# Optimization experiments

Measured on AMD Instinct MI355X. Metric: run time of the kernel, lower is better.

Reference implementation:

```python
import jax, jax.numpy as jnp
import numpy as np

M = 16384          # test points
N = 16384          # train points
D = 2              # (kx, ky)
CHUNK = 8192       # rows of K_star per chunk (matches torch default)


def setup_inputs() -> dict:
    key = jax.random.key(0)
    k1, k2, k3 = jax.random.split(key, 3)
    X_test = jax.random.normal(k1, (M, D), dtype=jnp.float32)
    X_train = jax.random.normal(k2, (N, D), dtype=jnp.float32)
    alpha = jax.random.normal(k3, (N, 2), dtype=jnp.float32)  # dual vars [Re, Im]
    log_lengthscale = jnp.asarray(np.log(0.1), dtype=jnp.float32)
    log_outputscale = jnp.asarray(np.log(1.0), dtype=jnp.float32)
    return {
        "X_test": X_test,
        "X_train": X_train,
        "alpha": alpha,
        "log_lengthscale": log_lengthscale,
        "log_outputscale": log_outputscale,
    }


def reference(X_test, X_train, alpha, log_lengthscale, log_outputscale):
    """Posterior mean mu* = K_rbf(X_test, X_train) @ alpha, chunked over test rows."""
    ell2 = jnp.exp(log_lengthscale) ** 2
    sf2 = jnp.exp(log_outputscale) ** 2
    xt_sq = jnp.sum(X_train * X_train, axis=1)  # (N,)

    def chunk_fn(xc):  # xc: (CHUNK, D)
        # squared euclidean distances (clamped at 0 for numerical safety)
        sq = (jnp.sum(xc * xc, axis=1)[:, None]
              + xt_sq[None, :]
              - 2.0 * (xc @ X_train.T))          # (CHUNK, N)
        sq = jnp.maximum(sq, 0.0)
        K = sf2 * jnp.exp(-0.5 * sq / ell2)      # RBF kernel values
        return K @ alpha                          # (CHUNK, 2)

    m = X_test.shape[0]
    chunks = X_test.reshape(m // CHUNK, CHUNK, D)
    out = jax.lax.map(chunk_fn, chunks)           # (m//CHUNK, CHUNK, 2)
    return out.reshape(m, 2)
```

## Files before the change

kernel.cpp:

```cpp
#include <hip/hip_runtime.h>
#include <math.h>

#define M_PTS 16384
#define N_PTS 16384

#define NC 42
#define NCELLS (NC * NC)
#define NPAIR (NCELLS / 2)
#define H 0.25f
#define INV_H 4.0f
#define ORIG (-5.25f)
#define TCUT 20.0f
#define KMAX 7
#define MAXROWS 16
#define NWAVES (M_PTS / 64)
#define CHUNK 1024
#define MAX_ITEMS 4096

#define OFF_NITEMS 0
#define OFF_TRCUR 64
#define OFF_TECUR (OFF_TRCUR + NCELLS * 4)
#define OFF_SROW  (OFF_TECUR + NCELLS * 4)
#define OFF_SPRE  (OFF_SROW + NWAVES * MAXROWS * 4)
#define OFF_ITEMS (OFF_SPRE + NWAVES * (MAXROWS + 1) * 4)
#define OFF_TRA   ((OFF_ITEMS + MAX_ITEMS * 4 + 255) & ~255)
#define OFF_TRW1  (OFF_TRA + N_PTS * 16)
#define OFF_T4    (OFF_TRW1 + N_PTS * 4)
#define WS_NEED   (OFF_T4 + (size_t)M_PTS * 16)

__device__ __forceinline__ float fexp2(float x) {
#if __has_builtin(__builtin_amdgcn_exp2f)
    return __builtin_amdgcn_exp2f(x);
#else
    return exp2f(x);
#endif
}

__device__ __forceinline__ void gatomic_fadd(float* p, float v) {
    asm volatile("global_atomic_add_f32 %0, %1, off" :: "v"(p), "v"(v) : "memory");
}

__device__ __forceinline__ int cellco(float v) {
    int c = (int)floorf((v - ORIG) * INV_H);
    return min(NC - 1, max(0, c));
}

__global__ __launch_bounds__(1024) void prep_kernel(
        const float2* __restrict__ Xtr, const float2* __restrict__ Xte,
        const float* __restrict__ log_ell,
        int* __restrict__ trcur, int* __restrict__ tecur,
        int* __restrict__ sRowG, int* __restrict__ sPreG,
        int* __restrict__ items, int* __restrict__ nitemsG) {
    __shared__ int hTr[NCELLS], hTe[NCELLS];
    __shared__ int sc[1024];
    __shared__ int trsL[NCELLS + 1], PL[NCELLS + 1];
    const int tid = threadIdx.x;

    if (tid == 0) nitemsG[0] = 0;
    for (int i = tid; i < NCELLS; i += 1024) { hTr[i] = 0; hTe[i] = 0; }
    __syncthreads();
    for (int i = tid; i < N_PTS; i += 1024) {
        float2 t = Xtr[i];
        atomicAdd(&hTr[cellco(t.y) * NC + cellco(t.x)], 1);
        float2 x = Xte[i];
        atomicAdd(&hTe[cellco(x.y) * NC + cellco(x.x)], 1);
    }
    __syncthreads();

    int pv = (tid < NPAIR) ? (hTr[2 * tid] + hTr[2 * tid + 1]) : 0;
    sc[tid] = pv; __syncthreads();
    for (int off = 1; off < 1024; off <<= 1) {
        int u = (tid >= off) ? sc[tid - off] : 0;
        __syncthreads(); sc[tid] += u; __syncthreads();
    }
    if (tid < NPAIR) {
        int e = sc[tid] - pv;
        trsL[2 * tid] = e;
        trsL[2 * tid + 1] = e + hTr[2 * tid];
    }
    if (tid == NPAIR - 1) trsL[NCELLS] = sc[tid];
    __syncthreads();

    pv = (tid < NPAIR) ? (hTe[2 * tid] + hTe[2 * tid + 1]) : 0;
    sc[tid] = pv; __syncthreads();
    for (int off = 1; off < 1024; off <<= 1) {
        int u = (tid >= off) ? sc[tid - off] : 0;
        __syncthreads(); sc[tid] += u; __syncthreads();
    }
    if (tid < NPAIR) {
        int e = sc[tid] - pv;
        PL[2 * tid] = e;
        PL[2 * tid + 1] = e + hTe[2 * tid];
    }
    if (tid == NPAIR - 1) PL[NCELLS] = sc[tid];
    __syncthreads();

    for (int c = tid; c < NCELLS; c += 1024) {
        trcur[c] = trsL[c];
        tecur[c] = PL[c];
    }

    if (tid < NWAVES) {
        const int w = tid;
        const float ell = expf(log_ell[0]);
        const float cmag = 0.5f / (ell * ell) * 1.4426950408889634f;
        const float r2 = TCUT / cmag;
        const int K = (int)floorf(sqrtf(r2) * INV_H) + 1;

        int clo, chi;
        {
            int s = w * 64, lo = 0, hi = NCELLS;
            while (lo + 1 < hi) { int m = (lo + hi) >> 1; if (PL[m] <= s) lo = m; else hi = m; }
            clo = lo;
            s = w * 64 + 63; lo = 0; hi = NCELLS;
            while (lo + 1 < hi) { int m = (lo + hi) >> 1; if (PL[m] <= s) lo = m; else hi = m; }
            chi = lo;
        }
        const int rl = clo / NC, cl = clo % NC;
        const int rh = chi / NC, ch = chi % NC;
        int wlo = max(0, rl - K), whi = min(NC - 1, rh + K);
        int nr = whi - wlo + 1;
        bool full = (K > KMAX) || (nr > MAXROWS);

        int pre = 0;
        if (full) {
            sRowG[w * MAXROWS] = 0;
            sPreG[w * (MAXROWS + 1)] = 0;
            pre = N_PTS;
            for (int i = 1; i <= MAXROWS; ++i) sPreG[w * (MAXROWS + 1) + i] = N_PTS;
        } else {
            const bool single = (rl == rh);
            const int cmin = single ? cl : 0;
            const int cmax = single ? ch : (NC - 1);
            sPreG[w * (MAXROWS + 1)] = 0;
            int idx = 0;
            for (int wr = wlo; wr <= whi; ++wr, ++idx) {
                int dy = (wr < rl) ? (rl - wr) : ((wr > rh) ? (wr - rh) : 0);
                int kx;
                if (dy <= 1) kx = K;
                else {
                    float d = (float)(dy - 1) * H;
                    kx = (int)floorf(sqrtf(fmaxf(r2 - d * d, 0.f)) * INV_H) + 1;
                }
                int c0 = max(0, cmin - kx);
                int c1 = min(NC - 1, cmax + kx);
                int js = trsL[wr * NC + c0];
                int je = trsL[wr * NC + c1 + 1];
                sRowG[w * MAXROWS + idx] = js - pre;
                pre += je - js;
                sPreG[w * (MAXROWS + 1) + idx + 1] = pre;
            }
            for (; idx < MAXROWS; ++idx)
                sPreG[w * (MAXROWS + 1) + idx + 1] = pre;
        }
        const int nch = (pre + CHUNK - 1) / CHUNK;
        for (int k = 0; k < nch; ++k) {
            int slot = atomicAdd(nitemsG, 1);
            items[slot] = w | (k << 16);
        }
    }
}

__global__ void scatter_kernel(const float2* __restrict__ Xtr,
                               const float2* __restrict__ Xte,
                               const float2* __restrict__ alpha,
                               const float* __restrict__ log_ell,
                               const float* __restrict__ log_sf,
                               int* __restrict__ trcur, int* __restrict__ tecur,
                               float4* __restrict__ trA, float* __restrict__ trW1,
                               float4* __restrict__ T4, float2* __restrict__ out2) {
    int i = blockIdx.x * blockDim.x + threadIdx.x;
    if (i >= N_PTS) return;
    out2[i] = make_float2(0.f, 0.f);
    float ell = expf(log_ell[0]);
    float sf2 = expf(2.0f * log_sf[0]);
    float c = -0.5f / (ell * ell) * 1.4426950408889634f;

    float2 t = Xtr[i];
    float2 a = alpha[i];
    int ct = cellco(t.y) * NC + cellco(t.x);
    int pt = atomicAdd(&trcur[ct], 1);
    trA[pt] = make_float4(-2.f * c * t.x, -2.f * c * t.y,
                          c * (t.x * t.x + t.y * t.y), sf2 * a.x);
    trW1[pt] = sf2 * a.y;

    float2 x = Xte[i];
    int cx = cellco(x.y) * NC + cellco(x.x);
    int px = atomicAdd(&tecur[cx], 1);
    T4[px] = make_float4(x.x, x.y, c * (x.x * x.x + x.y * x.y),
                         __int_as_float(i));
}

__global__ __launch_bounds__(256) void gp_main(
        const float4* __restrict__ T4, const float4* __restrict__ trA,
        const float* __restrict__ trW1, const int* __restrict__ sRowG,
        const int* __restrict__ sPreG, const int* __restrict__ items,
        const int* __restrict__ nitemsG, float* __restrict__ out) {
    const int nit = nitemsG[0];
    if ((int)blockIdx.x >= nit) return;
    const int item = items[blockIdx.x];
    const int w = item & 0xFFFF;
    const int k = item >> 16;

    __shared__ float4 sA[CHUNK];
    __shared__ __align__(16) float sW[CHUNK];
    __shared__ float2 red[4][64];
    __shared__ int off[MAXROWS];
    __shared__ int pre[MAXROWS + 1];

    const int tid = threadIdx.x;
    const int p = tid >> 6;
    const int lane = tid & 63;

    if (tid < MAXROWS) off[tid] = sRowG[w * MAXROWS + tid];
    if (tid < MAXROWS + 1) pre[tid] = sPreG[w * (MAXROWS + 1) + tid];

    float4 tp = T4[w * 64 + lane];
    const float x = tp.x, y = tp.y, b = tp.z;
    const int oi = __float_as_int(tp.w);
    __syncthreads();

    const int total = pre[MAXROWS];
    const int base0 = k << 10;
    const int n = min(CHUNK, total - base0);

    {
        int r = 0;
        for (int g = tid; g < CHUNK; g += 256) {
            float4 tv; float wv;
            if (g < n) {
                int gg = base0 + g;
                while (gg >= pre[r + 1]) ++r;
                int j = gg + off[r];
                tv = trA[j];
                wv = trW1[j];
            } else {
                tv = make_float4(0.f, 0.f, -1.0e30f, 0.f);
                wv = 0.f;
            }
            sA[g] = tv;
            sW[g] = wv;
        }
    }
    __syncthreads();

    float a0 = 0.f, a1 = 0.f;
#pragma unroll 2
    for (int q = p; q < CHUNK / 4; q += 4) {
        float4 t0 = sA[4 * q];
        float4 t1 = sA[4 * q + 1];
        float4 t2 = sA[4 * q + 2];
        float4 t3 = sA[4 * q + 3];
        float4 wv = *(const float4*)&sW[4 * q];
        float e0 = fexp2(fmaf(t0.x, x, fmaf(t0.y, y, b + t0.z)));
        float e1 = fexp2(fmaf(t1.x, x, fmaf(t1.y, y, b + t1.z)));
        float e2 = fexp2(fmaf(t2.x, x, fmaf(t2.y, y, b + t2.z)));
        float e3 = fexp2(fmaf(t3.x, x, fmaf(t3.y, y, b + t3.z)));
        a0 = fmaf(e0, t0.w, a0); a1 = fmaf(e0, wv.x, a1);
        a0 = fmaf(e1, t1.w, a0); a1 = fmaf(e1, wv.y, a1);
        a0 = fmaf(e2, t2.w, a0); a1 = fmaf(e2, wv.z, a1);
        a0 = fmaf(e3, t3.w, a0); a1 = fmaf(e3, wv.w, a1);
    }

    red[p][lane] = make_float2(a0, a1);
    __syncthreads();
    if (p == 0) {
        float s0 = 0.f, s1 = 0.f;
#pragma unroll
        for (int q = 0; q < 4; ++q) {
            float2 v = red[q][lane];
            s0 += v.x; s1 += v.y;
        }
        if (s0 != 0.f || s1 != 0.f) {
            gatomic_fadd(&out[2 * oi], s0);
            gatomic_fadd(&out[2 * oi + 1], s1);
        }
    }
}

__global__ __launch_bounds__(256, 8) void gp_dense(
        const float2* __restrict__ Xte, const float2* __restrict__ Xtr,
        const float2* __restrict__ alpha, const float* __restrict__ log_ell,
        const float* __restrict__ log_sf, float* __restrict__ out) {
    __shared__ float4 sSt[128];
    __shared__ float sA1[128];
    const int tid = threadIdx.x;
    const float ell = expf(log_ell[0]);
    const float c = -0.5f / (ell * ell) * 1.4426950408889634f;
    const int j0 = blockIdx.y * 128;
    if (tid < 128) {
        const float sf2 = expf(2.0f * log_sf[0]);
        float2 t = Xtr[j0 + tid];
        float2 a = alpha[j0 + tid];
        sSt[tid] = make_float4(-2.f * c * t.x, -2.f * c * t.y,
                               c * (t.x * t.x + t.y * t.y), sf2 * a.x);
        sA1[tid] = sf2 * a.y;
    }
    const int base = blockIdx.x * 1024 + tid;
    float2 x0 = Xte[base], x1 = Xte[base + 256];
    float2 x2 = Xte[base + 512], x3 = Xte[base + 768];
    const float b0 = c * (x0.x * x0.x + x0.y * x0.y);
    const float b1 = c * (x1.x * x1.x + x1.y * x1.y);
    const float b2 = c * (x2.x * x2.x + x2.y * x2.y);
    const float b3 = c * (x3.x * x3.x + x3.y * x3.y);
    __syncthreads();
    float a00 = 0.f, a01 = 0.f, a10 = 0.f, a11 = 0.f;
    float a20 = 0.f, a21 = 0.f, a30 = 0.f, a31 = 0.f;
#pragma unroll 2
    for (int j = 0; j < 128; ++j) {
        float4 s = sSt[j];
        float w1 = sA1[j];
        float e0 = fexp2(fminf(fmaf(s.x, x0.x, fmaf(s.y, x0.y, b0 + s.z)), 0.f));
        float e1 = fexp2(fminf(fmaf(s.x, x1.x, fmaf(s.y, x1.y, b1 + s.z)), 0.f));
        float e2 = fexp2(fminf(fmaf(s.x, x2.x, fmaf(s.y, x2.y, b2 + s.z)), 0.f));
        float e3 = fexp2(fminf(fmaf(s.x, x3.x, fmaf(s.y, x3.y, b3 + s.z)), 0.f));
        a00 = fmaf(e0, s.w, a00); a01 = fmaf(e0, w1, a01);
        a10 = fmaf(e1, s.w, a10); a11 = fmaf(e1, w1, a11);
        a20 = fmaf(e2, s.w, a20); a21 = fmaf(e2, w1, a21);
        a30 = fmaf(e3, s.w, a30); a31 = fmaf(e3, w1, a31);
    }
    gatomic_fadd(&out[2 * base], a00);            gatomic_fadd(&out[2 * base + 1], a01);
    gatomic_fadd(&out[2 * (base + 256)], a10);    gatomic_fadd(&out[2 * (base + 256) + 1], a11);
    gatomic_fadd(&out[2 * (base + 512)], a20);    gatomic_fadd(&out[2 * (base + 512) + 1], a21);
    gatomic_fadd(&out[2 * (base + 768)], a30);    gatomic_fadd(&out[2 * (base + 768) + 1], a31);
}

extern "C" void kernel_launch(void* const* d_in, const int* in_sizes, int n_in,
                              void* d_out, int out_size, void* d_ws, size_t ws_size,
                              hipStream_t stream) {
    const float2* Xte = (const float2*)d_in[0];
    const float2* Xtr = (const float2*)d_in[1];
    const float2* alpha = (const float2*)d_in[2];
    const float* log_ell = (const float*)d_in[3];
    const float* log_sf = (const float*)d_in[4];
    float* out = (float*)d_out;

    if (ws_size >= WS_NEED) {
        char* ws = (char*)d_ws;
        int* nitems = (int*)(ws + OFF_NITEMS);
        int* trcur = (int*)(ws + OFF_TRCUR);
        int* tecur = (int*)(ws + OFF_TECUR);
        int* sRowG = (int*)(ws + OFF_SROW);
        int* sPreG = (int*)(ws + OFF_SPRE);
        int* items = (int*)(ws + OFF_ITEMS);
        float4* trA = (float4*)(ws + OFF_TRA);
        float* trW1 = (float*)(ws + OFF_TRW1);
        float4* T4 = (float4*)(ws + OFF_T4);

        prep_kernel<<<1, 1024, 0, stream>>>(Xtr, Xte, log_ell, trcur, tecur,
                                            sRowG, sPreG, items, nitems);
        scatter_kernel<<<N_PTS / 256, 256, 0, stream>>>(
            Xtr, Xte, alpha, log_ell, log_sf, trcur, tecur, trA, trW1, T4,
            (float2*)out);
        gp_main<<<MAX_ITEMS, 256, 0, stream>>>(T4, trA, trW1, sRowG, sPreG,
                                               items, nitems, out);
    } else {
        hipMemsetAsync(out, 0, (size_t)out_size * sizeof(float), stream);
        dim3 grid(M_PTS / 1024, N_PTS / 128);
        gp_dense<<<grid, 256, 0, stream>>>(Xte, Xtr, alpha, log_ell, log_sf, out);
    }
}
```

Baseline: 116.0 us.

## Fuse prep, scatter and main passes into one cooperative persistent kernel

```diff
diff --git a/kernel.cpp b/kernel.cpp
--- a/kernel.cpp
+++ b/kernel.cpp
@@ -1,12 +1,14 @@
 #include <hip/hip_runtime.h>
+#include <hip/hip_cooperative_groups.h>
 #include <math.h>
+
+namespace cg = cooperative_groups;
 
 #define M_PTS 16384
 #define N_PTS 16384
 
 #define NC 42
 #define NCELLS (NC * NC)
-#define NPAIR (NCELLS / 2)
 #define H 0.25f
 #define INV_H 4.0f
 #define ORIG (-5.25f)
@@ -16,9 +18,12 @@
 #define NWAVES (M_PTS / 64)
 #define CHUNK 1024
 #define MAX_ITEMS 4096
+#define GRID_F 512
 
 #define OFF_NITEMS 0
-#define OFF_TRCUR 64
+#define OFF_HTR   64
+#define OFF_HTE   (OFF_HTR + NCELLS * 4)
+#define OFF_TRCUR (OFF_HTE + NCELLS * 4)
 #define OFF_TECUR (OFF_TRCUR + NCELLS * 4)
 #define OFF_SROW  (OFF_TECUR + NCELLS * 4)
 #define OFF_SPRE  (OFF_SROW + NWAVES * MAXROWS * 4)
@@ -43,6 +48,260 @@
 __device__ __forceinline__ int cellco(float v) {
     int c = (int)floorf((v - ORIG) * INV_H);
     return min(NC - 1, max(0, c));
+}
+
+__global__ __launch_bounds__(256) void gp_fused(
+        const float2* __restrict__ Xte, const float2* __restrict__ Xtr,
+        const float2* __restrict__ alpha, const float* __restrict__ log_ell,
+        const float* __restrict__ log_sf, char* __restrict__ ws,
+        float* __restrict__ out) {
+    int* nitemsG = (int*)(ws + OFF_NITEMS);
+    int* hG      = (int*)(ws + OFF_HTR);
+    int* hTrG    = (int*)(ws + OFF_HTR);
+    int* hTeG    = (int*)(ws + OFF_HTE);
+    int* trcurG  = (int*)(ws + OFF_TRCUR);
+    int* tecurG  = (int*)(ws + OFF_TECUR);
+    int* sRowG   = (int*)(ws + OFF_SROW);
+    int* sPreG   = (int*)(ws + OFF_SPRE);
+    int* itemsG  = (int*)(ws + OFF_ITEMS);
+    float4* trA  = (float4*)(ws + OFF_TRA);
+    float* trW1  = (float*)(ws + OFF_TRW1);
+    float4* T4   = (float4*)(ws + OFF_T4);
+
+    cg::grid_group grid = cg::this_grid();
+
+    __shared__ union {
+        struct { int trsL[NCELLS + 1]; int PL[NCELLS + 1]; int sc[256]; } s;
+        struct { float4 sA[CHUNK]; float sW[CHUNK]; float2 red[4][64]; } m;
+    } u;
+    __shared__ int off[MAXROWS];
+    __shared__ int pre[MAXROWS + 1];
+
+    const int tid = threadIdx.x;
+    const int gtid = (int)blockIdx.x * 256 + tid;
+    const int gsz = GRID_F * 256;
+
+    for (int i = gtid; i < 2 * NCELLS; i += gsz) hG[i] = 0;
+    if (gtid == 0) nitemsG[0] = 0;
+    {
+        float4* o4 = (float4*)out;
+        for (int i = gtid; i < (M_PTS * 2) / 4; i += gsz)
+            o4[i] = make_float4(0.f, 0.f, 0.f, 0.f);
+    }
+    grid.sync();
+
+    for (int i = gtid; i < N_PTS; i += gsz) {
+        float2 t = Xtr[i];
+        atomicAdd(&hTrG[cellco(t.y) * NC + cellco(t.x)], 1);
+        float2 x = Xte[i];
+        atomicAdd(&hTeG[cellco(x.y) * NC + cellco(x.x)], 1);
+    }
+    grid.sync();
+
+    if (blockIdx.x == 0) {
+        {
+            int lo[7]; int s = 0;
+#pragma unroll
+            for (int k = 0; k < 7; ++k) {
+                int c = tid * 7 + k;
+                int v = (c < NCELLS) ? hTrG[c] : 0;
+                lo[k] = s; s += v;
+            }
+            u.s.sc[tid] = s; __syncthreads();
+            for (int o = 1; o < 256; o <<= 1) {
+                int t2 = (tid >= o) ? u.s.sc[tid - o] : 0;
+                __syncthreads(); u.s.sc[tid] += t2; __syncthreads();
+            }
+            int ex = u.s.sc[tid] - s;
+#pragma unroll
+            for (int k = 0; k < 7; ++k) {
+                int c = tid * 7 + k;
+                if (c < NCELLS) { int v = ex + lo[k]; u.s.trsL[c] = v; trcurG[c] = v; }
+            }
+            if (tid == 255) u.s.trsL[NCELLS] = u.s.sc[255];
+            __syncthreads();
+        }
+        {
+            int lo[7]; int s = 0;
+#pragma unroll
+            for (int k = 0; k < 7; ++k) {
+                int c = tid * 7 + k;
+                int v = (c < NCELLS) ? hTeG[c] : 0;
+                lo[k] = s; s += v;
+            }
+            u.s.sc[tid] = s; __syncthreads();
+            for (int o = 1; o < 256; o <<= 1) {
+                int t2 = (tid >= o) ? u.s.sc[tid - o] : 0;
+                __syncthreads(); u.s.sc[tid] += t2; __syncthreads();
+            }
+            int ex = u.s.sc[tid] - s;
+#pragma unroll
+            for (int k = 0; k < 7; ++k) {
+                int c = tid * 7 + k;
+                if (c < NCELLS) { int v = ex + lo[k]; u.s.PL[c] = v; tecurG[c] = v; }
+            }
+            if (tid == 255) u.s.PL[NCELLS] = u.s.sc[255];
+        }
+    }
+    grid.sync();
+
+    if (blockIdx.x == 0) {
+        const int w = tid;
+        const float ell = expf(log_ell[0]);
+        const float cmag = 0.5f / (ell * ell) * 1.4426950408889634f;
+        const float r2 = TCUT / cmag;
+        const int K = (int)floorf(sqrtf(r2) * INV_H) + 1;
+
+        int clo, chi;
+        {
+            int s = w * 64, lo = 0, hi = NCELLS;
+            while (lo + 1 < hi) { int m = (lo + hi) >> 1; if (u.s.PL[m] <= s) lo = m; else hi = m; }
+            clo = lo;
+            s = w * 64 + 63; lo = 0; hi = NCELLS;
+            while (lo + 1 < hi) { int m = (lo + hi) >> 1; if (u.s.PL[m] <= s) lo = m; else hi = m; }
+            chi = lo;
+        }
+        const int rl = clo / NC, cl = clo % NC;
+        const int rh = chi / NC, ch = chi % NC;
+        int wlo = max(0, rl - K), whi = min(NC - 1, rh + K);
+        int nr = whi - wlo + 1;
+        bool full = (K > KMAX) || (nr > MAXROWS);
+
+        int prw = 0;
+        if (full) {
+            sRowG[w * MAXROWS] = 0;
+            sPreG[w * (MAXROWS + 1)] = 0;
+            prw = N_PTS;
+            for (int i = 1; i <= MAXROWS; ++i) sPreG[w * (MAXROWS + 1) + i] = N_PTS;
+        } else {
+            const bool single = (rl == rh);
+            const int cmin = single ? cl : 0;
+            const int cmax = single ? ch : (NC - 1);
+            sPreG[w * (MAXROWS + 1)] = 0;
+            int idx = 0;
+            for (int wr = wlo; wr <= whi; ++wr, ++idx) {
+                int dy = (wr < rl) ? (rl - wr) : ((wr > rh) ? (wr - rh) : 0);
+                int kx;
+                if (dy <= 1) kx = K;
+                else {
+                    float d = (float)(dy - 1) * H;
+                    kx = (int)floorf(sqrtf(fmaxf(r2 - d * d, 0.f)) * INV_H) + 1;
+                }
+                int c0 = max(0, cmin - kx);
+                int c1 = min(NC - 1, cmax + kx);
+                int js = u.s.trsL[wr * NC + c0];
+                int je = u.s.trsL[wr * NC + c1 + 1];
+                sRowG[w * MAXROWS + idx] = js - prw;
+                prw += je - js;
+                sPreG[w * (MAXROWS + 1) + idx + 1] = prw;
+            }
+            for (; idx < MAXROWS; ++idx)
+                sPreG[w * (MAXROWS + 1) + idx + 1] = prw;
+        }
+        const int nch = (prw + CHUNK - 1) / CHUNK;
+        for (int k = 0; k < nch; ++k) {
+            int slot = atomicAdd(nitemsG, 1);
+            itemsG[slot] = w | (k << 16);
+        }
+    } else {
+        int i = ((int)blockIdx.x - 1) * 256 + tid;
+        if (i < N_PTS) {
+            float ell = expf(log_ell[0]);
+            float sf2 = expf(2.0f * log_sf[0]);
+            float c = -0.5f / (ell * ell) * 1.4426950408889634f;
+
+            float2 t = Xtr[i];
+            float2 a = alpha[i];
+            int ct = cellco(t.y) * NC + cellco(t.x);
+            int pt = atomicAdd(&trcurG[ct], 1);
+            trA[pt] = make_float4(-2.f * c * t.x, -2.f * c * t.y,
+                                  c * (t.x * t.x + t.y * t.y), sf2 * a.x);
+            trW1[pt] = sf2 * a.y;
+
+            float2 x = Xte[i];
+            int cx = cellco(x.y) * NC + cellco(x.x);
+            int px = atomicAdd(&tecurG[cx], 1);
+            T4[px] = make_float4(x.x, x.y, c * (x.x * x.x + x.y * x.y),
+                                 __int_as_float(i));
+        }
+    }
+    grid.sync();
+
+    const int p = tid >> 6;
+    const int lane = tid & 63;
+    const int nit = nitemsG[0];
+
+    for (int ib = (int)blockIdx.x; ib < nit; ib += GRID_F) {
+        const int item = itemsG[ib];
+        const int w = item & 0xFFFF;
+        const int k = item >> 16;
+
+        if (tid < MAXROWS) off[tid] = sRowG[w * MAXROWS + tid];
+        if (tid < MAXROWS + 1) pre[tid] = sPreG[w * (MAXROWS + 1) + tid];
+
+        float4 tp = T4[w * 64 + lane];
+        const float x = tp.x, y = tp.y, b = tp.z;
+        const int oi = __float_as_int(tp.w);
+        __syncthreads();
+
+        const int total = pre[MAXROWS];
+        const int base0 = k << 10;
+        const int n = min(CHUNK, total - base0);
+
+        {
+            int r = 0;
+            for (int g = tid; g < CHUNK; g += 256) {
+                float4 tv; float wv;
+                if (g < n) {
+                    int gg = base0 + g;
+                    while (gg >= pre[r + 1]) ++r;
+                    int j = gg + off[r];
+                    tv = trA[j];
+                    wv = trW1[j];
+                } else {
+                    tv = make_float4(0.f, 0.f, -1.0e30f, 0.f);
+                    wv = 0.f;
+                }
+                u.m.sA[g] = tv;
+                u.m.sW[g] = wv;
+            }
+        }
+        __syncthreads();
+
+        float a0 = 0.f, a1 = 0.f;
+#pragma unroll 2
+        for (int q = p; q < CHUNK / 4; q += 4) {
+            float4 t0 = u.m.sA[4 * q];
+            float4 t1 = u.m.sA[4 * q + 1];
+            float4 t2 = u.m.sA[4 * q + 2];
+            float4 t3 = u.m.sA[4 * q + 3];
+            float4 wv = *(const float4*)&u.m.sW[4 * q];
+            float e0 = fexp2(fmaf(t0.x, x, fmaf(t0.y, y, b + t0.z)));
+            float e1 = fexp2(fmaf(t1.x, x, fmaf(t1.y, y, b + t1.z)));
+            float e2 = fexp2(fmaf(t2.x, x, fmaf(t2.y, y, b + t2.z)));
+            float e3 = fexp2(fmaf(t3.x, x, fmaf(t3.y, y, b + t3.z)));
+            a0 = fmaf(e0, t0.w, a0); a1 = fmaf(e0, wv.x, a1);
+            a0 = fmaf(e1, t1.w, a0); a1 = fmaf(e1, wv.y, a1);
+            a0 = fmaf(e2, t2.w, a0); a1 = fmaf(e2, wv.z, a1);
+            a0 = fmaf(e3, t3.w, a0); a1 = fmaf(e3, wv.w, a1);
+        }
+
+        u.m.red[p][lane] = make_float2(a0, a1);
+        __syncthreads();
+        if (p == 0) {
+            float s0 = 0.f, s1 = 0.f;
+#pragma unroll
+            for (int q = 0; q < 4; ++q) {
+                float2 v = u.m.red[q][lane];
+                s0 += v.x; s1 += v.y;
+            }
+            if (s0 != 0.f || s1 != 0.f) {
+                gatomic_fadd(&out[2 * oi], s0);
+                gatomic_fadd(&out[2 * oi + 1], s1);
+            }
+        }
+        __syncthreads();
+    }
 }
 
 __global__ __launch_bounds__(1024) void prep_kernel(
@@ -67,32 +326,32 @@
     }
     __syncthreads();
 
-    int pv = (tid < NPAIR) ? (hTr[2 * tid] + hTr[2 * tid + 1]) : 0;
+    int pv = (tid < NCELLS / 2) ? (hTr[2 * tid] + hTr[2 * tid + 1]) : 0;
     sc[tid] = pv; __syncthreads();
     for (int off = 1; off < 1024; off <<= 1) {
         int u = (tid >= off) ? sc[tid - off] : 0;
         __syncthreads(); sc[tid] += u; __syncthreads();
     }
-    if (tid < NPAIR) {
+    if (tid < NCELLS / 2) {
         int e = sc[tid] - pv;
         trsL[2 * tid] = e;
         trsL[2 * tid + 1] = e + hTr[2 * tid];
     }
-    if (tid == NPAIR - 1) trsL[NCELLS] = sc[tid];
-    __syncthreads();
-
-    pv = (tid < NPAIR) ? (hTe[2 * tid] + hTe[2 * tid + 1]) : 0;
+    if (tid == NCELLS / 2 - 1) trsL[NCELLS] = sc[tid];
+    __syncthreads();
+
+    pv = (tid < NCELLS / 2) ? (hTe[2 * tid] + hTe[2 * tid + 1]) : 0;
     sc[tid] = pv; __syncthreads();
     for (int off = 1; off < 1024; off <<= 1) {
         int u = (tid >= off) ? sc[tid - off] : 0;
         __syncthreads(); sc[tid] += u; __syncthreads();
     }
-    if (tid < NPAIR) {
+    if (tid < NCELLS / 2) {
         int e = sc[tid] - pv;
         PL[2 * tid] = e;
         PL[2 * tid + 1] = e + hTe[2 * tid];
     }
-    if (tid == NPAIR - 1) PL[NCELLS] = sc[tid];
+    if (tid == NCELLS / 2 - 1) PL[NCELLS] = sc[tid];
     __syncthreads();
 
     for (int c = tid; c < NCELLS; c += 1024) {
@@ -122,11 +381,11 @@
         int nr = whi - wlo + 1;
         bool full = (K > KMAX) || (nr > MAXROWS);
 
-        int pre = 0;
+        int prw = 0;
         if (full) {
             sRowG[w * MAXROWS] = 0;
             sPreG[w * (MAXROWS + 1)] = 0;
-            pre = N_PTS;
+            prw = N_PTS;
             for (int i = 1; i <= MAXROWS; ++i) sPreG[w * (MAXROWS + 1) + i] = N_PTS;
         } else {
             const bool single = (rl == rh);
@@ -146,14 +405,14 @@
                 int c1 = min(NC - 1, cmax + kx);
                 int js = trsL[wr * NC + c0];
                 int je = trsL[wr * NC + c1 + 1];
-                sRowG[w * MAXROWS + idx] = js - pre;
-                pre += je - js;
-                sPreG[w * (MAXROWS + 1) + idx + 1] = pre;
+                sRowG[w * MAXROWS + idx] = js - prw;
+                prw += je - js;
+                sPreG[w * (MAXROWS + 1) + idx + 1] = prw;
             }
             for (; idx < MAXROWS; ++idx)
-                sPreG[w * (MAXROWS + 1) + idx + 1] = pre;
-        }
-        const int nch = (pre + CHUNK - 1) / CHUNK;
+                sPreG[w * (MAXROWS + 1) + idx + 1] = prw;
+        }
+        const int nch = (prw + CHUNK - 1) / CHUNK;
         for (int k = 0; k < nch; ++k) {
             int slot = atomicAdd(nitemsG, 1);
             items[slot] = w | (k << 16);
@@ -337,23 +596,30 @@
 
     if (ws_size >= WS_NEED) {
         char* ws = (char*)d_ws;
-        int* nitems = (int*)(ws + OFF_NITEMS);
-        int* trcur = (int*)(ws + OFF_TRCUR);
-        int* tecur = (int*)(ws + OFF_TECUR);
-        int* sRowG = (int*)(ws + OFF_SROW);
-        int* sPreG = (int*)(ws + OFF_SPRE);
-        int* items = (int*)(ws + OFF_ITEMS);
-        float4* trA = (float4*)(ws + OFF_TRA);
-        float* trW1 = (float*)(ws + OFF_TRW1);
-        float4* T4 = (float4*)(ws + OFF_T4);
-
-        prep_kernel<<<1, 1024, 0, stream>>>(Xtr, Xte, log_ell, trcur, tecur,
-                                            sRowG, sPreG, items, nitems);
-        scatter_kernel<<<N_PTS / 256, 256, 0, stream>>>(
-            Xtr, Xte, alpha, log_ell, log_sf, trcur, tecur, trA, trW1, T4,
-            (float2*)out);
-        gp_main<<<MAX_ITEMS, 256, 0, stream>>>(T4, trA, trW1, sRowG, sPreG,
-                                               items, nitems, out);
+        void* kargs[] = {(void*)&Xte, (void*)&Xtr, (void*)&alpha,
+                         (void*)&log_ell, (void*)&log_sf, (void*)&ws,
+                         (void*)&out};
+        hipError_t err = hipLaunchCooperativeKernel(
+            (void*)gp_fused, dim3(GRID_F), dim3(256), kargs, 0, stream);
+        if (err != hipSuccess) {
+            int* nitems = (int*)(ws + OFF_NITEMS);
+            int* trcur = (int*)(ws + OFF_TRCUR);
+            int* tecur = (int*)(ws + OFF_TECUR);
+            int* sRowG = (int*)(ws + OFF_SROW);
+            int* sPreG = (int*)(ws + OFF_SPRE);
+            int* items = (int*)(ws + OFF_ITEMS);
+            float4* trA = (float4*)(ws + OFF_TRA);
+            float* trW1 = (float*)(ws + OFF_TRW1);
+            float4* T4 = (float4*)(ws + OFF_T4);
+
+            prep_kernel<<<1, 1024, 0, stream>>>(Xtr, Xte, log_ell, trcur, tecur,
+                                                sRowG, sPreG, items, nitems);
+            scatter_kernel<<<N_PTS / 256, 256, 0, stream>>>(
+                Xtr, Xte, alpha, log_ell, log_sf, trcur, tecur, trA, trW1, T4,
+                (float2*)out);
+            gp_main<<<MAX_ITEMS, 256, 0, stream>>>(T4, trA, trW1, sRowG, sPreG,
+                                                   items, nitems, out);
+        }
     } else {
         hipMemsetAsync(out, 0, (size_t)out_size * sizeof(float), stream);
         dim3 grid(M_PTS / 1024, N_PTS / 128);
```

After: 321.5 us. 177% more time.
